# Optimization experiments

Measured on AMD Instinct MI355X. Metric: run time of the kernel, lower is better.

The kernel has to match this reference:

```python
import jax, jax.numpy as jnp
import numpy as np

ALPHA = 0.2  # LeakyReLU negative slope
NEG_INF = -9e15


def setup_inputs() -> dict:
    key = jax.random.key(0)
    ks = jax.random.split(key, 12)
    Nd, Nk = 8000, 2000
    Fd, Fk, H, Hh = 32, 16, 64, 8
    s = lambda fan_in: 1.0 / np.sqrt(fan_in)
    return {
        "raw_drone": jax.random.normal(ks[0], (Nd, Fd), jnp.float32),
        "raw_dock": jax.random.normal(ks[1], (Nk, Fk), jnp.float32),
        "adj": jax.random.randint(ks[2], (Nd, Nk), 0, 2, jnp.int32),
        # proj_drone / proj_dock (nn.Linear)
        "Wpd": jax.random.uniform(ks[3], (Fd, H), jnp.float32, -s(Fd), s(Fd)),
        "bpd": jnp.zeros((H,), jnp.float32),
        "Wpk": jax.random.uniform(ks[4], (Fk, H), jnp.float32, -s(Fk), s(Fk)),
        "bpk": jnp.zeros((H,), jnp.float32),
        # per-head GAT params, stacked over heads: W [Hh,H,H], attention vecs a1,a2 [Hh,H]
        "Wa": jax.random.uniform(ks[5], (Hh, H, H), jnp.float32, -s(H), s(H)),
        "a1": jax.random.uniform(ks[6], (Hh, H), jnp.float32, -s(H), s(H)),
        "a2": jax.random.uniform(ks[7], (Hh, H), jnp.float32, -s(H), s(H)),
        # feature_fusion (nn.Linear nhid*nheads -> nhid)
        "Wf": jax.random.uniform(ks[8], (Hh * H, H), jnp.float32, -s(Hh * H), s(Hh * H)),
        "bf": jnp.zeros((H,), jnp.float32),
    }


def reference(raw_drone, raw_dock, adj, Wpd, bpd, Wpk, bpk, Wa, a1, a2, Wf, bf):
    # input projections + ELU (dropout is identity in eval mode)
    h_drone = jax.nn.elu(raw_drone @ Wpd + bpd)  # [Nd, H]
    h_dock = jax.nn.elu(raw_dock @ Wpk + bpk)    # [Nk, H]

    # per-head linear transforms, vectorized over heads
    Whd = jnp.einsum("nd,hdf->hnf", h_drone, Wa)  # [Hh, Nd, F]
    Whk = jnp.einsum("kd,hdf->hkf", h_dock, Wa)   # [Hh, Nk, F]

    # additive GAT scores: e[h,n,k] = LeakyReLU(a1_h . Whd[h,n] + a2_h . Whk[h,k])
    sd = jnp.einsum("hnf,hf->hn", Whd, a1)  # [Hh, Nd]
    sk = jnp.einsum("hkf,hf->hk", Whk, a2)  # [Hh, Nk]
    e = jax.nn.leaky_relu(sd[:, :, None] + sk[:, None, :], negative_slope=ALPHA)

    # adjacency-masked softmax over dock axis
    e = jnp.where(adj[None, :, :] > 0, e, NEG_INF)
    attn = jax.nn.softmax(e, axis=-1)  # [Hh, Nd, Nk]

    # aggregate dock features, ELU (concat=True), concat heads
    hp = jax.nn.elu(jnp.einsum("hnk,hkf->hnf", attn, Whk))  # [Hh, Nd, F]
    Nd = hp.shape[1]
    hp = jnp.transpose(hp, (1, 0, 2)).reshape(Nd, -1)  # [Nd, Hh*F]

    out_drone = hp @ Wf + bf
    return (out_drone, h_dock)
```

## Files before the change

### kernel.cpp

```cpp
#include <hip/hip_runtime.h>
#include <stdint.h>

#define Nd 8000
#define Nk 2000
#define FD 32
#define FK 16
#define HD 64
#define NH 8
#define KP 2048
#define NKB 64
#define LOG2E 1.44269504088896f
#define NSLOPE 0.2f

typedef float f4 __attribute__((ext_vector_type(4)));
typedef short s16x8 __attribute__((ext_vector_type(8)));
typedef int i4 __attribute__((ext_vector_type(4)));
typedef unsigned int u32;
typedef unsigned short u16;
typedef unsigned int u4v __attribute__((ext_vector_type(4)));

#define WS_WHKB   0
#define WS_SK     2097152
#define WS_SD     2162688
#define WS_ADJB   2418688
#define WS_WFT    4466688
#define WS_HP     4532224

__device__ inline u16 f2bf_rne(float f){
  u32 u = __float_as_uint(f);
  u32 r = u + 0x7fffu + ((u >> 16) & 1u);
  return (u16)(r >> 16);
}
__device__ inline float elu1(float x){
  return x > 0.f ? x : (__builtin_amdgcn_exp2f(x * LOG2E) - 1.f);
}

__global__ __launch_bounds__(256) void k_prep(const float* __restrict__ rdrone,
                                              const float* __restrict__ rdock,
                                              const int*   __restrict__ adj,
                                              const float* __restrict__ Wpd,
                                              const float* __restrict__ bpd,
                                              const float* __restrict__ Wpk,
                                              const float* __restrict__ bpk,
                                              const float* __restrict__ Wa,
                                              const float* __restrict__ a1,
                                              const float* __restrict__ a2,
                                              const float* __restrict__ Wf,
                                              float* __restrict__ out_hdock,
                                              u16* __restrict__ whkB,
                                              float* __restrict__ sk,
                                              float* __restrict__ sd,
                                              u32* __restrict__ adjb,
                                              u16* __restrict__ wfT){
  __shared__ __align__(16) char smem[13440];
  int b = blockIdx.x;
  int t = threadIdx.x;

  if (b < 2000) {
    int W = b * 256 + t;
    int n = W >> 6, c = W & 63;
    int k0 = c * 32;
    const int* rowp = adj + n * Nk;
    u32 bits = 0;
    #pragma unroll
    for (int q = 0; q < 8; ++q) {
      int kq = min(k0 + q * 4, Nk - 4);
      i4 v = *(const i4*)(rowp + kq);
      bits |= (v[0] != 0 ? 1u : 0u) << (q * 4);
      bits |= (v[1] != 0 ? 1u : 0u) << (q * 4 + 1);
      bits |= (v[2] != 0 ? 1u : 0u) << (q * 4 + 2);
      bits |= (v[3] != 0 ? 1u : 0u) << (q * 4 + 3);
    }
    int rem = Nk - k0;
    u32 tm = (rem >= 32) ? 0xFFFFFFFFu : ((rem <= 0) ? 0u : ((1u << rem) - 1u));
    adjb[W] = bits & tm;
    return;
  }
  if (b < 2512) {
    int idx = b - 2000;
    int kt = idx & 63, h = idx >> 6;
    float* hs   = (float*)smem;
    float* part = (float*)(smem + 8320);
    u16*   ts   = (u16*)(smem + 9344);
    if (h == 1) {
      int id = kt * 256 + t;
      #pragma unroll
      for (int i = 0; i < 2; ++i) {
        int ix = id * 2 + i;
        int j = ix >> 9, k = ix & 511;
        wfT[ix] = f2bf_rne(Wf[k * HD + j]);
      }
    }
    {
      int r = t >> 3, f0 = (t & 7) * 8;
      int gk = kt * 32 + r;
      float v[8];
      if (gk < Nk) {
        #pragma unroll
        for (int q = 0; q < 8; ++q) v[q] = bpk[f0 + q];
        for (int j = 0; j < FK; ++j) {
          float x = rdock[gk * FK + j];
          #pragma unroll
          for (int q = 0; q < 8; ++q) v[q] += x * Wpk[j * HD + f0 + q];
        }
        #pragma unroll
        for (int q = 0; q < 8; ++q) v[q] = elu1(v[q]);
        if (h == 0) {
          #pragma unroll
          for (int q = 0; q < 8; ++q) out_hdock[gk * HD + f0 + q] = v[q];
        }
      } else {
        #pragma unroll
        for (int q = 0; q < 8; ++q) v[q] = 0.f;
      }
      #pragma unroll
      for (int q = 0; q < 8; ++q) hs[r * 65 + f0 + q] = v[q];
    }
    __syncthreads();
    {
      int kl = t & 31, fq = t >> 5;
      float acc[8];
      #pragma unroll
      for (int j = 0; j < 8; ++j) acc[j] = 0.f;
      for (int d = 0; d < HD; ++d) {
        float hv = hs[kl * 65 + d];
        const float* wr = Wa + (h * HD + d) * HD + fq * 8;
        #pragma unroll
        for (int j = 0; j < 8; ++j) acc[j] += hv * wr[j];
      }
      float ps = 0.f;
      #pragma unroll
      for (int j = 0; j < 8; ++j) ps += acc[j] * a2[h * HD + fq * 8 + j];
      part[kl * 8 + fq] = ps;
      #pragma unroll
      for (int j = 0; j < 8; ++j)
        ts[(fq * 8 + j) * 32 + kl] = f2bf_rne(acc[j]);
    }
    __syncthreads();
    if (t < 32) {
      float s = 0.f;
      #pragma unroll
      for (int q = 0; q < 8; ++q) s += part[t * 8 + q];
      sk[h * KP + kt * 32 + t] = s * LOG2E;
    }
    {
      int cc = t >> 6, lane = t & 63, g = (t >> 4) & 3, c16 = t & 15;
      int f = cc * 16 + c16;
      u4v val = *(const u4v*)&ts[f * 32 + g * 8];
      *(u4v*)(whkB + (((h * NKB + kt) * 4 + cc) * 64 + lane) * 8) = val;
    }
    return;
  }
  {
    int bid = b - 2512;
    float* wa1 = (float*)smem;
    #pragma unroll
    for (int i = 0; i < 2; ++i) {
      int ix = t + i * 256;
      int h = ix >> 6, d = ix & 63;
      float s = 0.f;
      for (int f = 0; f < HD; ++f) s += Wa[(h * HD + d) * HD + f] * a1[h * HD + f];
      wa1[ix] = s;
    }
    __syncthreads();
    int r4 = t >> 6, d = t & 63;
    for (int rr = 0; rr < 4; ++rr) {
      int n = bid * 16 + r4 * 4 + rr;
      float acc = bpd[d];
      for (int j = 0; j < FD; ++j) acc += rdrone[n * FD + j] * Wpd[j * HD + d];
      float hd = elu1(acc);
      #pragma unroll
      for (int h = 0; h < NH; ++h) {
        float v = hd * wa1[h * HD + d];
        v += __shfl_xor(v, 1);  v += __shfl_xor(v, 2);  v += __shfl_xor(v, 4);
        v += __shfl_xor(v, 8);  v += __shfl_xor(v, 16); v += __shfl_xor(v, 32);
        if (d == 0) sd[h * Nd + n] = v * LOG2E;
      }
    }
  }
}

__global__ __launch_bounds__(256) void k_attn(const float* __restrict__ sd,
                                              const float* __restrict__ sk,
                                              const u16* __restrict__ whkB,
                                              const u32* __restrict__ adjb,
                                              u16* __restrict__ hp){
  int bid = blockIdx.x;
  int h = bid & 7, nt = bid >> 3;
  int t = threadIdx.x;
  int w = t >> 6, lane = t & 63, g = lane >> 4, c16 = lane & 15;
  int r0 = nt * 128 + w * 32;
  __shared__ u16 ldshp[128 * 64];

  int rowA[2]; float sdv[2];
  #pragma unroll
  for (int m = 0; m < 2; ++m) {
    rowA[m] = min(r0 + m * 16 + c16, Nd - 1);
    sdv[m] = sd[h * Nd + rowA[m]];
  }
  f4 acc[2][4], accd[2];
  #pragma unroll
  for (int m = 0; m < 2; ++m) {
    accd[m] = (f4){0.f, 0.f, 0.f, 0.f};
    #pragma unroll
    for (int cc = 0; cc < 4; ++cc) acc[m][cc] = (f4){0.f, 0.f, 0.f, 0.f};
  }
  s16x8 onesf = (s16x8)(short)((c16 == 0) ? 0x3F80 : 0);

  const u16* bb = whkB + h * (NKB * 4 * 64 * 8);
  const float* skh = sk + h * KP;
  const u32* ap0 = adjb + rowA[0] * 64;
  const u32* ap1 = adjb + rowA[1] * 64;

  s16x8 cb0, cb1, cb2, cb3;
  {
    const u16* bp = bb + lane * 8;
    cb0 = *(const s16x8*)(bp);
    cb1 = *(const s16x8*)(bp + 512);
    cb2 = *(const s16x8*)(bp + 1024);
    cb3 = *(const s16x8*)(bp + 1536);
  }
  f4 cs0 = *(const f4*)(skh + g * 8);
  f4 cs1 = *(const f4*)(skh + g * 8 + 4);
  u4v caw0 = *(const u4v*)(ap0);
  u4v caw1 = *(const u4v*)(ap1);

  for (int kb4 = 0; kb4 < 16; ++kb4) {
    u4v naw0 = *(const u4v*)(ap0 + kb4 * 4 + 4);
    u4v naw1 = *(const u4v*)(ap1 + kb4 * 4 + 4);
    #pragma unroll
    for (int u = 0; u < 4; ++u) {
      int kb = kb4 * 4 + u;
      const u16* np = bb + (kb + 1) * 2048 + lane * 8;
      s16x8 nb0 = *(const s16x8*)(np);
      s16x8 nb1 = *(const s16x8*)(np + 512);
      s16x8 nb2 = *(const s16x8*)(np + 1024);
      s16x8 nb3 = *(const s16x8*)(np + 1536);
      const float* nsp = skh + (kb + 1) * 32 + g * 8;
      f4 ns0 = *(const f4*)nsp;
      f4 ns1 = *(const f4*)(nsp + 4);

      u32 awm0 = caw0[u], awm1 = caw1[u];
      union { s16x8 v; u32 d[4]; } af[2];
      #pragma unroll
      for (int m = 0; m < 2; ++m) {
        u32 ab = ((m ? awm1 : awm0) >> (g * 8)) & 0xffu;
        f4 x0 = cs0 + sdv[m];
        f4 x1 = cs1 + sdv[m];
        x0 = __builtin_elementwise_max(x0, x0 * NSLOPE);
        x1 = __builtin_elementwise_max(x1, x1 * NSLOPE);
        float p[8];
        #pragma unroll
        for (int e = 0; e < 4; ++e) {
          p[e]     = __builtin_amdgcn_exp2f(x0[e]);
          p[e + 4] = __builtin_amdgcn_exp2f(x1[e]);
        }
        #pragma unroll
        for (int e = 0; e < 8; ++e) {
          int mk = __builtin_amdgcn_sbfe(ab, e, 1);
          p[e] = __uint_as_float(__float_as_uint(p[e]) & (u32)mk);
        }
        #pragma unroll
        for (int jj = 0; jj < 4; ++jj)
          asm("v_cvt_pk_bf16_f32 %0, %1, %2"
              : "=v"(af[m].d[jj]) : "v"(p[2 * jj]), "v"(p[2 * jj + 1]));
      }
      #pragma unroll
      for (int m = 0; m < 2; ++m) {
        accd[m]   = __builtin_amdgcn_mfma_f32_16x16x32_bf16(af[m].v, onesf, accd[m], 0, 0, 0);
        acc[m][0] = __builtin_amdgcn_mfma_f32_16x16x32_bf16(af[m].v, cb0, acc[m][0], 0, 0, 0);
        acc[m][1] = __builtin_amdgcn_mfma_f32_16x16x32_bf16(af[m].v, cb1, acc[m][1], 0, 0, 0);
        acc[m][2] = __builtin_amdgcn_mfma_f32_16x16x32_bf16(af[m].v, cb2, acc[m][2], 0, 0, 0);
        acc[m][3] = __builtin_amdgcn_mfma_f32_16x16x32_bf16(af[m].v, cb3, acc[m][3], 0, 0, 0);
      }
      cb0 = nb0; cb1 = nb1; cb2 = nb2; cb3 = nb3;
      cs0 = ns0; cs1 = ns1;
    }
    caw0 = naw0; caw1 = naw1;
  }

  #pragma unroll
  for (int m = 0; m < 2; ++m) {
    #pragma unroll
    for (int j = 0; j < 4; ++j) {
      float den = __shfl(accd[m][j], lane & 48);
      int row = r0 + m * 16 + g * 4 + j;
      float linv = (row < Nd && den > 0.f) ? 1.f / den : 0.f;
      #pragma unroll
      for (int cc = 0; cc < 4; ++cc) {
        float o = acc[m][cc][j] * linv;
        ldshp[(w * 32 + m * 16 + g * 4 + j) * 64 + cc * 16 + c16] = f2bf_rne(elu1(o));
      }
    }
  }
  __syncthreads();
  {
    int r = t >> 1, half = t & 1;
    int row = nt * 128 + r;
    if (row < Nd) {
      u16* dst = hp + row * 512 + h * 64 + half * 32;
      const u16* src = ldshp + r * 64 + half * 32;
      *(u4v*)(dst)      = *(const u4v*)(src);
      *(u4v*)(dst + 8)  = *(const u4v*)(src + 8);
      *(u4v*)(dst + 16) = *(const u4v*)(src + 16);
      *(u4v*)(dst + 24) = *(const u4v*)(src + 24);
    }
  }
}

__global__ __launch_bounds__(256) void k_out(const u16* __restrict__ hp,
                                             const u16* __restrict__ wfT,
                                             const float* __restrict__ bfv,
                                             float* __restrict__ out){
  int t = threadIdx.x;
  int w = t >> 6, lane = t & 63, g = lane >> 4, c16 = lane & 15;
  int r0 = blockIdx.x * 16;
  f4 acc = (f4){0.f, 0.f, 0.f, 0.f};
  const u16* ap = hp + (r0 + c16) * 512 + g * 8;
  const u16* bp = wfT + (w * 16 + c16) * 512 + g * 8;
  #pragma unroll 4
  for (int kb = 0; kb < 16; ++kb) {
    s16x8 a = *(const s16x8*)(ap + kb * 32);
    s16x8 b = *(const s16x8*)(bp + kb * 32);
    acc = __builtin_amdgcn_mfma_f32_16x16x32_bf16(a, b, acc, 0, 0, 0);
  }
  float bias = bfv[w * 16 + c16];
  #pragma unroll
  for (int j = 0; j < 4; ++j)
    out[(r0 + g * 4 + j) * HD + w * 16 + c16] = acc[j] + bias;
}

extern "C" void kernel_launch(void* const* d_in, const int* in_sizes, int n_in,
                              void* d_out, int out_size, void* d_ws, size_t ws_size,
                              hipStream_t stream) {
  const float* raw_drone = (const float*)d_in[0];
  const float* raw_dock  = (const float*)d_in[1];
  const int*   adj       = (const int*)d_in[2];
  const float* Wpd = (const float*)d_in[3];
  const float* bpd = (const float*)d_in[4];
  const float* Wpk = (const float*)d_in[5];
  const float* bpk = (const float*)d_in[6];
  const float* Wa  = (const float*)d_in[7];
  const float* a1  = (const float*)d_in[8];
  const float* a2  = (const float*)d_in[9];
  const float* Wf  = (const float*)d_in[10];
  const float* bfb = (const float*)d_in[11];
  float* out = (float*)d_out;
  float* out_hdock = out + Nd * HD;

  char* ws = (char*)d_ws;
  u16*   whkB = (u16*)(ws + WS_WHKB);
  float* skv  = (float*)(ws + WS_SK);
  float* sdv  = (float*)(ws + WS_SD);
  u32*   adjb = (u32*)(ws + WS_ADJB);
  u16*   wfT  = (u16*)(ws + WS_WFT);
  u16*   hp   = (u16*)(ws + WS_HP);

  k_prep<<<3012, 256, 0, stream>>>(raw_drone, raw_dock, adj, Wpd, bpd, Wpk, bpk,
                                   Wa, a1, a2, Wf, out_hdock, whkB, skv, sdv,
                                   adjb, wfT);
  k_attn<<<504, 256, 0, stream>>>(sdv, skv, whkB, adjb, hp);
  k_out <<<500, 256, 0, stream>>>(hp, wfT, bfb, out);
}
```

Measured before the change: 108.2 us.

## Stage Whk tiles through double-buffered LDS and split adjacency packing kernel

The attention kernel no longer has every wave load the full 2048-element B tile from global memory. The four waves now cooperatively stage each tile into a double-buffered shared-memory slot, with a one-step register prefetch, and read operands from LDS. This cuts redundant global and L2 traffic by about a factor of four, at the cost of one block barrier per k-step. Separately, adjacency bit-packing moves into its own kernel where each thread packs two words. This adds a launch but makes the prep kernel's block mix less heterogeneous.

```diff
diff --git a/kernel.cpp b/kernel.cpp
--- a/kernel.cpp
+++ b/kernel.cpp
@@ -35,9 +35,38 @@
   return x > 0.f ? x : (__builtin_amdgcn_exp2f(x * LOG2E) - 1.f);
 }
 
+__global__ __launch_bounds__(256) void k_adjb(const int* __restrict__ adj,
+                                              u32* __restrict__ adjb){
+  int id = blockIdx.x * 256 + threadIdx.x;
+  int w0 = id * 2;
+  int n = w0 >> 6, c0 = w0 & 63;
+  int k0 = c0 * 32;
+  const int* rowp = adj + n * Nk;
+  u32 b0 = 0, b1 = 0;
+  #pragma unroll
+  for (int q = 0; q < 8; ++q) {
+    int ka = min(k0 + q * 4, Nk - 4);
+    int kb = min(k0 + 32 + q * 4, Nk - 4);
+    i4 va = *(const i4*)(rowp + ka);
+    i4 vb = *(const i4*)(rowp + kb);
+    b0 |= (va[0] != 0 ? 1u : 0u) << (q * 4);
+    b0 |= (va[1] != 0 ? 1u : 0u) << (q * 4 + 1);
+    b0 |= (va[2] != 0 ? 1u : 0u) << (q * 4 + 2);
+    b0 |= (va[3] != 0 ? 1u : 0u) << (q * 4 + 3);
+    b1 |= (vb[0] != 0 ? 1u : 0u) << (q * 4);
+    b1 |= (vb[1] != 0 ? 1u : 0u) << (q * 4 + 1);
+    b1 |= (vb[2] != 0 ? 1u : 0u) << (q * 4 + 2);
+    b1 |= (vb[3] != 0 ? 1u : 0u) << (q * 4 + 3);
+  }
+  int r0 = Nk - k0, r1 = Nk - k0 - 32;
+  u32 t0 = (r0 >= 32) ? 0xFFFFFFFFu : ((r0 <= 0) ? 0u : ((1u << r0) - 1u));
+  u32 t1 = (r1 >= 32) ? 0xFFFFFFFFu : ((r1 <= 0) ? 0u : ((1u << r1) - 1u));
+  adjb[w0]     = b0 & t0;
+  adjb[w0 + 1] = b1 & t1;
+}
+
 __global__ __launch_bounds__(256) void k_prep(const float* __restrict__ rdrone,
                                               const float* __restrict__ rdock,
-                                              const int*   __restrict__ adj,
                                               const float* __restrict__ Wpd,
                                               const float* __restrict__ bpd,
                                               const float* __restrict__ Wpk,
@@ -50,35 +79,13 @@
                                               u16* __restrict__ whkB,
                                               float* __restrict__ sk,
                                               float* __restrict__ sd,
-                                              u32* __restrict__ adjb,
                                               u16* __restrict__ wfT){
   __shared__ __align__(16) char smem[13440];
   int b = blockIdx.x;
   int t = threadIdx.x;
 
-  if (b < 2000) {
-    int W = b * 256 + t;
-    int n = W >> 6, c = W & 63;
-    int k0 = c * 32;
-    const int* rowp = adj + n * Nk;
-    u32 bits = 0;
-    #pragma unroll
-    for (int q = 0; q < 8; ++q) {
-      int kq = min(k0 + q * 4, Nk - 4);
-      i4 v = *(const i4*)(rowp + kq);
-      bits |= (v[0] != 0 ? 1u : 0u) << (q * 4);
-      bits |= (v[1] != 0 ? 1u : 0u) << (q * 4 + 1);
-      bits |= (v[2] != 0 ? 1u : 0u) << (q * 4 + 2);
-      bits |= (v[3] != 0 ? 1u : 0u) << (q * 4 + 3);
-    }
-    int rem = Nk - k0;
-    u32 tm = (rem >= 32) ? 0xFFFFFFFFu : ((rem <= 0) ? 0u : ((1u << rem) - 1u));
-    adjb[W] = bits & tm;
-    return;
-  }
-  if (b < 2512) {
-    int idx = b - 2000;
-    int kt = idx & 63, h = idx >> 6;
+  if (b < 512) {
+    int kt = b & 63, h = b >> 6;
     float* hs   = (float*)smem;
     float* part = (float*)(smem + 8320);
     u16*   ts   = (u16*)(smem + 9344);
@@ -152,7 +159,7 @@
     return;
   }
   {
-    int bid = b - 2512;
+    int bid = b - 512;
     float* wa1 = (float*)smem;
     #pragma unroll
     for (int i = 0; i < 2; ++i) {
@@ -190,6 +197,7 @@
   int t = threadIdx.x;
   int w = t >> 6, lane = t & 63, g = lane >> 4, c16 = lane & 15;
   int r0 = nt * 128 + w * 32;
+  __shared__ u16 bslot[2][2048];
   __shared__ u16 ldshp[128 * 64];
 
   int rowA[2]; float sdv[2];
@@ -211,19 +219,15 @@
   const float* skh = sk + h * KP;
   const u32* ap0 = adjb + rowA[0] * 64;
   const u32* ap1 = adjb + rowA[1] * 64;
-
-  s16x8 cb0, cb1, cb2, cb3;
-  {
-    const u16* bp = bb + lane * 8;
-    cb0 = *(const s16x8*)(bp);
-    cb1 = *(const s16x8*)(bp + 512);
-    cb2 = *(const s16x8*)(bp + 1024);
-    cb3 = *(const s16x8*)(bp + 1536);
-  }
+  int soff = w * 512 + lane * 8;
+
+  *(u4v*)&bslot[0][soff] = *(const u4v*)(bb + soff);
+  u4v stag = *(const u4v*)(bb + 2048 + soff);
   f4 cs0 = *(const f4*)(skh + g * 8);
   f4 cs1 = *(const f4*)(skh + g * 8 + 4);
   u4v caw0 = *(const u4v*)(ap0);
   u4v caw1 = *(const u4v*)(ap1);
+  __syncthreads();
 
   for (int kb4 = 0; kb4 < 16; ++kb4) {
     u4v naw0 = *(const u4v*)(ap0 + kb4 * 4 + 4);
@@ -231,11 +235,8 @@
     #pragma unroll
     for (int u = 0; u < 4; ++u) {
       int kb = kb4 * 4 + u;
-      const u16* np = bb + (kb + 1) * 2048 + lane * 8;
-      s16x8 nb0 = *(const s16x8*)(np);
-      s16x8 nb1 = *(const s16x8*)(np + 512);
-      s16x8 nb2 = *(const s16x8*)(np + 1024);
-      s16x8 nb3 = *(const s16x8*)(np + 1536);
+      u4v nx;
+      if (kb < 62) nx = *(const u4v*)(bb + (kb + 2) * 2048 + soff);
       const float* nsp = skh + (kb + 1) * 32 + g * 8;
       f4 ns0 = *(const f4*)nsp;
       f4 ns1 = *(const f4*)(nsp + 4);
@@ -265,15 +266,21 @@
           asm("v_cvt_pk_bf16_f32 %0, %1, %2"
               : "=v"(af[m].d[jj]) : "v"(p[2 * jj]), "v"(p[2 * jj + 1]));
       }
+      __syncthreads();
+      if (kb < 63) *(u4v*)&bslot[(kb + 1) & 1][soff] = stag;
+      s16x8 b0 = *(const s16x8*)&bslot[kb & 1][lane * 8];
+      s16x8 b1 = *(const s16x8*)&bslot[kb & 1][512 + lane * 8];
+      s16x8 b2 = *(const s16x8*)&bslot[kb & 1][1024 + lane * 8];
+      s16x8 b3 = *(const s16x8*)&bslot[kb & 1][1536 + lane * 8];
       #pragma unroll
       for (int m = 0; m < 2; ++m) {
         accd[m]   = __builtin_amdgcn_mfma_f32_16x16x32_bf16(af[m].v, onesf, accd[m], 0, 0, 0);
-        acc[m][0] = __builtin_amdgcn_mfma_f32_16x16x32_bf16(af[m].v, cb0, acc[m][0], 0, 0, 0);
-        acc[m][1] = __builtin_amdgcn_mfma_f32_16x16x32_bf16(af[m].v, cb1, acc[m][1], 0, 0, 0);
-        acc[m][2] = __builtin_amdgcn_mfma_f32_16x16x32_bf16(af[m].v, cb2, acc[m][2], 0, 0, 0);
-        acc[m][3] = __builtin_amdgcn_mfma_f32_16x16x32_bf16(af[m].v, cb3, acc[m][3], 0, 0, 0);
-      }
-      cb0 = nb0; cb1 = nb1; cb2 = nb2; cb3 = nb3;
+        acc[m][0] = __builtin_amdgcn_mfma_f32_16x16x32_bf16(af[m].v, b0, acc[m][0], 0, 0, 0);
+        acc[m][1] = __builtin_amdgcn_mfma_f32_16x16x32_bf16(af[m].v, b1, acc[m][1], 0, 0, 0);
+        acc[m][2] = __builtin_amdgcn_mfma_f32_16x16x32_bf16(af[m].v, b2, acc[m][2], 0, 0, 0);
+        acc[m][3] = __builtin_amdgcn_mfma_f32_16x16x32_bf16(af[m].v, b3, acc[m][3], 0, 0, 0);
+      }
+      stag = nx;
       cs0 = ns0; cs1 = ns1;
     }
     caw0 = naw0; caw1 = naw1;
@@ -356,9 +363,9 @@
   u16*   wfT  = (u16*)(ws + WS_WFT);
   u16*   hp   = (u16*)(ws + WS_HP);
 
-  k_prep<<<3012, 256, 0, stream>>>(raw_drone, raw_dock, adj, Wpd, bpd, Wpk, bpk,
-                                   Wa, a1, a2, Wf, out_hdock, whkB, skv, sdv,
-                                   adjb, wfT);
+  k_adjb<<<1000, 256, 0, stream>>>(adj, adjb);
+  k_prep<<<1012, 256, 0, stream>>>(raw_drone, raw_dock, Wpd, bpd, Wpk, bpk,
+                                   Wa, a1, a2, Wf, out_hdock, whkB, skv, sdv, wfT);
   k_attn<<<504, 256, 0, stream>>>(sdv, skv, whkB, adjb, hp);
   k_out <<<500, 256, 0, stream>>>(hp, wfT, bfb, out);
 }
```

Result: slower. 112.1 us (+3.6%).
